# Kernel optimization log

Measured on AMD Instinct MI355X. Metric: run time of the kernel, lower is better.

Reference implementation:

```python
import jax, jax.numpy as jnp
import numpy as np

N_NODES = 500000
D_FEAT = 128
BATCH = 16384
K_NEIGH = 32
N_MASKS = 4  # module hardcodes 4 masks with exponents 0.5*j (gcn path)


def setup_inputs() -> dict:
    key = jax.random.key(0)
    k1, k2, k3 = jax.random.split(key, 3)
    embed = jax.random.normal(k1, (N_NODES, D_FEAT), dtype=jnp.float32)
    neigh_idx = jax.random.randint(k2, (BATCH, K_NEIGH), 0, N_NODES, dtype=jnp.int32)
    # positive weights (original uses 1+degree counts; any positive weight is valid)
    neigh_w = jax.random.uniform(k3, (BATCH, K_NEIGH), dtype=jnp.float32, minval=0.05, maxval=1.0)
    return {"embed": embed, "neigh_idx": neigh_idx, "neigh_w": neigh_w}


def reference(embed, neigh_idx, neigh_w):
    # gather neighbor features: [B, K, d] (the sparse equivalent of mask.mm(embed_matrix))
    feats = embed[neigh_idx]
    # exponents 0.5*j for j = 0..3 (gcn=True branch: pow(node_weight, 0.5*j))
    exps = 0.5 * jnp.arange(N_MASKS, dtype=neigh_w.dtype)  # [4]
    W = neigh_w[None, :, :] ** exps[:, None, None]          # [4, B, K]
    # row-normalize each mask (mask.div(mask.sum(1, keepdim=True)))
    Wn = W / jnp.sum(W, axis=-1, keepdims=True)
    # weighted aggregation per mask: [4, B, d]
    out = jnp.einsum('jbk,bkd->jbd', Wn, feats)
    # concat the 4 aggregations along feature dim -> [B, 4*d]
    B = feats.shape[0]
    return jnp.moveaxis(out, 0, 1).reshape(B, N_MASKS * D_FEAT)
```

## Files before the change

### kernel.cpp

```cpp
#include <hip/hip_runtime.h>
#include <math.h>

#define BATCH 16384
#define KN 32
#define DF 128
#define NM 4

__global__ __launch_bounds__(128) void wagg_kernel(
    const float* __restrict__ embed,
    const int*   __restrict__ nidx,
    const float* __restrict__ nw,
    float*       __restrict__ out)
{
    const int b = blockIdx.x;
    const int t = threadIdx.x;

    __shared__ float wn[NM][KN];
    __shared__ int   sidx[KN];

    if (t < KN) {
        const float wv = nw[b * KN + t];
        const float sq = sqrtf(wv);
        wn[0][t] = 1.0f;
        wn[1][t] = sq;
        wn[2][t] = wv;
        wn[3][t] = wv * sq;
        sidx[t]  = nidx[b * KN + t];
    }
    __syncthreads();

    float inv[NM];
    #pragma unroll
    for (int j = 0; j < NM; ++j) {
        float s = 0.0f;
        #pragma unroll
        for (int k = 0; k < KN; ++k) s += wn[j][k];
        inv[j] = 1.0f / s;
    }

    const int f  = t & 31;
    const int kb = t >> 5;

    float4 acc[NM];
    #pragma unroll
    for (int j = 0; j < NM; ++j) { acc[j].x = acc[j].y = acc[j].z = acc[j].w = 0.0f; }

    #pragma unroll
    for (int kk = 0; kk < 8; ++kk) {
        const int k = kb * 8 + kk;
        const size_t row = (size_t)sidx[k];
        const float4 v = *((const float4*)(embed + row * DF) + f);
        #pragma unroll
        for (int j = 0; j < NM; ++j) {
            const float wj = wn[j][k];
            acc[j].x += wj * v.x;
            acc[j].y += wj * v.y;
            acc[j].z += wj * v.z;
            acc[j].w += wj * v.w;
        }
    }

    __shared__ float4 part[4][NM][32];
    #pragma unroll
    for (int j = 0; j < NM; ++j) part[kb][j][f] = acc[j];
    __syncthreads();

    const int jo = t >> 5;
    float4 r;
    r.x = part[0][jo][f].x + part[1][jo][f].x + part[2][jo][f].x + part[3][jo][f].x;
    r.y = part[0][jo][f].y + part[1][jo][f].y + part[2][jo][f].y + part[3][jo][f].y;
    r.z = part[0][jo][f].z + part[1][jo][f].z + part[2][jo][f].z + part[3][jo][f].z;
    r.w = part[0][jo][f].w + part[1][jo][f].w + part[2][jo][f].w + part[3][jo][f].w;

    const float s = inv[jo];
    r.x *= s; r.y *= s; r.z *= s; r.w *= s;

    ((float4*)(out + (size_t)b * (NM * DF)))[t] = r;
}

extern "C" void kernel_launch(void* const* d_in, const int* in_sizes, int n_in,
                              void* d_out, int out_size, void* d_ws, size_t ws_size,
                              hipStream_t stream) {
    const float* embed = (const float*)d_in[0];
    const int*   nidx  = (const int*)  d_in[1];
    const float* nw    = (const float*)d_in[2];
    float* out = (float*)d_out;

    wagg_kernel<<<BATCH, 128, 0, stream>>>(embed, nidx, nw, out);
}
```

Measured before the change: 342.0 us.

## Map one 32-lane group per batch row, 8 rows per block, drop smem reduction

```diff
diff --git a/kernel.cpp b/kernel.cpp
--- a/kernel.cpp
+++ b/kernel.cpp
@@ -5,77 +5,78 @@
 #define KN 32
 #define DF 128
 #define NM 4
+#define RPB 8
 
-__global__ __launch_bounds__(128) void wagg_kernel(
+__global__ __launch_bounds__(256, 4) void wagg_kernel(
     const float* __restrict__ embed,
     const int*   __restrict__ nidx,
     const float* __restrict__ nw,
     float*       __restrict__ out)
 {
-    const int b = blockIdx.x;
-    const int t = threadIdx.x;
+    const int t  = threadIdx.x;
+    const int r  = t >> 5;
+    const int f  = t & 31;
+    const int b  = blockIdx.x * RPB + r;
 
-    __shared__ float wn[NM][KN];
-    __shared__ int   sidx[KN];
+    __shared__ float4 wq[RPB][KN];
+    __shared__ int    sidx[RPB][KN];
+    __shared__ float4 sinv[RPB];
 
-    if (t < KN) {
-        const float wv = nw[b * KN + t];
-        const float sq = sqrtf(wv);
-        wn[0][t] = 1.0f;
-        wn[1][t] = sq;
-        wn[2][t] = wv;
-        wn[3][t] = wv * sq;
-        sidx[t]  = nidx[b * KN + t];
+    {
+        const float w  = nw[(size_t)b * KN + f];
+        const float sq = sqrtf(w);
+        float4 q;
+        q.x = 1.0f; q.y = sq; q.z = w; q.w = w * sq;
+        wq[r][f]   = q;
+        sidx[r][f] = nidx[(size_t)b * KN + f];
+
+        float4 s = q;
+        #pragma unroll
+        for (int m = 1; m < 32; m <<= 1) {
+            s.x += __shfl_xor(s.x, m);
+            s.y += __shfl_xor(s.y, m);
+            s.z += __shfl_xor(s.z, m);
+            s.w += __shfl_xor(s.w, m);
+        }
+        if (f == 0) {
+            float4 iv;
+            iv.x = 1.0f / s.x;
+            iv.y = 1.0f / s.y;
+            iv.z = 1.0f / s.z;
+            iv.w = 1.0f / s.w;
+            sinv[r] = iv;
+        }
     }
     __syncthreads();
 
-    float inv[NM];
+    float4 a0, a1, a2, a3;
+    a0.x=a0.y=a0.z=a0.w=0.f;
+    a1.x=a1.y=a1.z=a1.w=0.f;
+    a2.x=a2.y=a2.z=a2.w=0.f;
+    a3.x=a3.y=a3.z=a3.w=0.f;
+
     #pragma unroll
-    for (int j = 0; j < NM; ++j) {
-        float s = 0.0f;
-        #pragma unroll
-        for (int k = 0; k < KN; ++k) s += wn[j][k];
-        inv[j] = 1.0f / s;
+    for (int k = 0; k < KN; ++k) {
+        const int    row = sidx[r][k];
+        const float4 q   = wq[r][k];
+        const float4 v   = *((const float4*)(embed + (size_t)row * DF) + f);
+        a0.x += v.x;        a0.y += v.y;        a0.z += v.z;        a0.w += v.w;
+        a1.x += q.y * v.x;  a1.y += q.y * v.y;  a1.z += q.y * v.z;  a1.w += q.y * v.w;
+        a2.x += q.z * v.x;  a2.y += q.z * v.y;  a2.z += q.z * v.z;  a2.w += q.z * v.w;
+        a3.x += q.w * v.x;  a3.y += q.w * v.y;  a3.z += q.w * v.z;  a3.w += q.w * v.w;
     }
 
-    const int f  = t & 31;
-    const int kb = t >> 5;
+    const float4 iv = sinv[r];
+    a0.x *= iv.x; a0.y *= iv.x; a0.z *= iv.x; a0.w *= iv.x;
+    a1.x *= iv.y; a1.y *= iv.y; a1.z *= iv.y; a1.w *= iv.y;
+    a2.x *= iv.z; a2.y *= iv.z; a2.z *= iv.z; a2.w *= iv.z;
+    a3.x *= iv.w; a3.y *= iv.w; a3.z *= iv.w; a3.w *= iv.w;
 
-    float4 acc[NM];
-    #pragma unroll
-    for (int j = 0; j < NM; ++j) { acc[j].x = acc[j].y = acc[j].z = acc[j].w = 0.0f; }
-
-    #pragma unroll
-    for (int kk = 0; kk < 8; ++kk) {
-        const int k = kb * 8 + kk;
-        const size_t row = (size_t)sidx[k];
-        const float4 v = *((const float4*)(embed + row * DF) + f);
-        #pragma unroll
-        for (int j = 0; j < NM; ++j) {
-            const float wj = wn[j][k];
-            acc[j].x += wj * v.x;
-            acc[j].y += wj * v.y;
-            acc[j].z += wj * v.z;
-            acc[j].w += wj * v.w;
-        }
-    }
-
-    __shared__ float4 part[4][NM][32];
-    #pragma unroll
-    for (int j = 0; j < NM; ++j) part[kb][j][f] = acc[j];
-    __syncthreads();
-
-    const int jo = t >> 5;
-    float4 r;
-    r.x = part[0][jo][f].x + part[1][jo][f].x + part[2][jo][f].x + part[3][jo][f].x;
-    r.y = part[0][jo][f].y + part[1][jo][f].y + part[2][jo][f].y + part[3][jo][f].y;
-    r.z = part[0][jo][f].z + part[1][jo][f].z + part[2][jo][f].z + part[3][jo][f].z;
-    r.w = part[0][jo][f].w + part[1][jo][f].w + part[2][jo][f].w + part[3][jo][f].w;
-
-    const float s = inv[jo];
-    r.x *= s; r.y *= s; r.z *= s; r.w *= s;
-
-    ((float4*)(out + (size_t)b * (NM * DF)))[t] = r;
+    float4* o = (float4*)(out + (size_t)b * (NM * DF));
+    o[0 * 32 + f] = a0;
+    o[1 * 32 + f] = a1;
+    o[2 * 32 + f] = a2;
+    o[3 * 32 + f] = a3;
 }
 
 extern "C" void kernel_launch(void* const* d_in, const int* in_sizes, int n_in,
@@ -86,5 +87,5 @@
     const float* nw    = (const float*)d_in[2];
     float* out = (float*)d_out;
 
-    wagg_kernel<<<BATCH, 128, 0, stream>>>(embed, nidx, nw, out);
+    wagg_kernel<<<BATCH / RPB, 256, 0, stream>>>(embed, nidx, nw, out);
 }
```

Result: no change. 339.5 us (-0.7%).
